# Performance work log

Measured on AMD Instinct MI355X. Metric: run time of the kernel, lower is better.

## Reference

```python
import jax, jax.numpy as jnp
import numpy as np


def _soft_attention(h, context, W_in, W_out):
    """Luong soft-dot attention. h: [B,H], context: [B,L,H].
    W_in: [H,H] (in,out layout), W_out: [2H,H]."""
    target = h @ W_in                                  # [B, H]
    attn = jnp.einsum('blh,bh->bl', context, target)   # [B, L]
    p = jax.nn.softmax(attn, axis=-1)                  # [B, L]
    weighted_ctx = jnp.einsum('bl,blh->bh', p, context)  # [B, H]
    h_tilde = jnp.tanh(jnp.concatenate([weighted_ctx, h], axis=1) @ W_out)  # [B, H]
    return h_tilde, p


def setup_inputs() -> dict:
    key = jax.random.key(0)
    ks = jax.random.split(key, 13)
    B, L, H = 64, 512, 1024
    s2 = 1.0 / np.sqrt(2 * H)
    s1 = 1.0 / np.sqrt(H)
    return {
        'h_tilde_s': jax.random.normal(ks[0], (B, H), jnp.float32),
        'h_tilde_o': jax.random.normal(ks[1], (B, H), jnp.float32),
        'h_tilde_a': jax.random.normal(ks[2], (B, H), jnp.float32),
        'enc_out': jax.random.normal(ks[3], (B, L, H), jnp.float32),
        'full_feature_len': 36,
        'W_as': jax.random.normal(ks[4], (2 * H, H), jnp.float32) * s2,
        'W_so': jax.random.normal(ks[5], (2 * H, H), jnp.float32) * s2,
        'W_oa': jax.random.normal(ks[6], (2 * H, H), jnp.float32) * s2,
        'Win_as': jax.random.normal(ks[7], (H, H), jnp.float32) * s1,
        'Win_so': jax.random.normal(ks[8], (H, H), jnp.float32) * s1,
        'Win_oa': jax.random.normal(ks[9], (H, H), jnp.float32) * s1,
        'Wout_as': jax.random.normal(ks[10], (2 * H, H), jnp.float32) * s2,
        'Wout_so': jax.random.normal(ks[11], (2 * H, H), jnp.float32) * s2,
        'Wout_oa': jax.random.normal(ks[12], (2 * H, H), jnp.float32) * s2,
    }


def reference(h_tilde_s, h_tilde_o, h_tilde_a, enc_out, full_feature_len,
              W_as, W_so, W_oa, Win_as, Win_so, Win_oa,
              Wout_as, Wout_so, Wout_oa):
    # Relational contexts via concat + linear(no bias) + tanh
    h_as = jnp.tanh(jnp.concatenate([h_tilde_a, h_tilde_s], axis=1) @ W_as)  # [B,H]
    h_so = jnp.tanh(jnp.concatenate([h_tilde_s, h_tilde_o], axis=1) @ W_so)
    h_oa = jnp.tanh(jnp.concatenate([h_tilde_o, h_tilde_a], axis=1) @ W_oa)
    # Three parallel soft-dot attentions over encoder output
    sa_as, _ = _soft_attention(h_as, enc_out, Win_as, Wout_as)
    sa_so, _ = _soft_attention(h_so, enc_out, Win_so, Wout_so)
    sa_oa, _ = _soft_attention(h_oa, enc_out, Win_oa, Wout_oa)
    B, H = sa_as.shape
    F = full_feature_len
    # repeat_interleave of size-1 dim == broadcast tile to [B, F, H]
    ctx_mas = jnp.broadcast_to(sa_as[:, None, :], (B, F, H))
    ctx_mso = jnp.broadcast_to(sa_so[:, None, :], (B, F, H))
    ctx_moa = jnp.broadcast_to(sa_oa[:, None, :], (B, F, H))
    return (ctx_mas, ctx_mso, ctx_moa)
```

## Files before the change

kernel.cpp:

```cpp
#include <hip/hip_runtime.h>

constexpr int BB = 64;
constexpr int LL = 512;
constexpr int HH = 1024;
constexpr int SPLITK = 4;

struct Ptr3 { const float* p[3]; };

template<int K0, int K1>
__global__ __launch_bounds__(256)
void gemm_skinny(Ptr3 A0, Ptr3 A1, Ptr3 Wp, float* __restrict__ part)
{
    constexpr int K = K0 + K1;
    constexpr int KRANGE = K / SPLITK;
    __shared__ float As[32][64];
    __shared__ float Ws[32][64];
    const int r   = blockIdx.z;
    const int n0  = blockIdx.x * 64;
    const int ks  = blockIdx.y * KRANGE;
    const int tid = threadIdx.x;
    const float* a0 = A0.p[r];
    const float* a1 = A1.p[r];
    const float* w  = Wp.p[r];

    const int tn = tid & 15;
    const int tm = tid >> 4;

    float acc[4][4] = {};

    for (int kt = ks; kt < ks + KRANGE; kt += 32) {
        {
            const int m   = tid >> 2;
            const int kk0 = (tid & 3) << 3;
            const int kg  = kt + kk0;
            const float* src = (kg < K0) ? (a0 + m * HH + kg)
                                         : (a1 + m * HH + (kg - K0));
            float4 v0 = *(const float4*)(src);
            float4 v1 = *(const float4*)(src + 4);
            As[kk0 + 0][m] = v0.x; As[kk0 + 1][m] = v0.y;
            As[kk0 + 2][m] = v0.z; As[kk0 + 3][m] = v0.w;
            As[kk0 + 4][m] = v1.x; As[kk0 + 5][m] = v1.y;
            As[kk0 + 6][m] = v1.z; As[kk0 + 7][m] = v1.w;
        }
        {
            const int j4 = (tid & 15) << 2;
            int kk = tid >> 4;
            #pragma unroll
            for (int i = 0; i < 2; i++, kk += 16) {
                *(float4*)&Ws[kk][j4] = *(const float4*)(w + (size_t)(kt + kk) * HH + n0 + j4);
            }
        }
        __syncthreads();
        #pragma unroll
        for (int kk = 0; kk < 32; kk++) {
            float4 a4 = *(const float4*)&As[kk][tm << 2];
            float4 b4 = *(const float4*)&Ws[kk][tn << 2];
            float av[4] = {a4.x, a4.y, a4.z, a4.w};
            float bv[4] = {b4.x, b4.y, b4.z, b4.w};
            #pragma unroll
            for (int i = 0; i < 4; i++)
                #pragma unroll
                for (int j = 0; j < 4; j++)
                    acc[i][j] += av[i] * bv[j];
        }
        __syncthreads();
    }

    float* dst = part + (size_t)((r * SPLITK + blockIdx.y) * 64) * HH + n0 + (tn << 2);
    #pragma unroll
    for (int i = 0; i < 4; i++) {
        const int m = (tm << 2) + i;
        *(float4*)(dst + (size_t)m * HH) = make_float4(acc[i][0], acc[i][1], acc[i][2], acc[i][3]);
    }
}

template<bool TANH>
__global__ __launch_bounds__(256)
void reduce_split(const float* __restrict__ part, float* __restrict__ dst)
{
    const int i4   = blockIdx.x * 256 + threadIdx.x;
    const int flat = i4 << 2;
    const int r    = flat >> 16;
    const int mn   = flat & 65535;
    const float* p = part + (size_t)r * SPLITK * 65536 + mn;
    float4 s = *(const float4*)p;
    #pragma unroll
    for (int y = 1; y < SPLITK; y++) {
        float4 q = *(const float4*)(p + (size_t)y * 65536);
        s.x += q.x; s.y += q.y; s.z += q.z; s.w += q.w;
    }
    if (TANH) {
        s.x = tanhf(s.x); s.y = tanhf(s.y); s.z = tanhf(s.z); s.w = tanhf(s.w);
    }
    *(float4*)(dst + (size_t)r * 65536 + mn) = s;
}

__global__ __launch_bounds__(256)
void attn_scores(const float* __restrict__ enc, const float* __restrict__ t,
                 float* __restrict__ attn)
{
    const int b    = blockIdx.x >> 4;
    const int lc   = blockIdx.x & 15;
    const int lane = threadIdx.x & 63;
    const int wave = threadIdx.x >> 6;

    float4 tr[3][4];
    #pragma unroll
    for (int r = 0; r < 3; r++)
        #pragma unroll
        for (int v = 0; v < 4; v++)
            tr[r][v] = *(const float4*)&t[(size_t)(r * BB + b) * HH + (lane << 2) + (v << 8)];

    const int lbase = (lc << 5) + (wave << 3);
    for (int i = 0; i < 8; i++) {
        const int l = lbase + i;
        const float* e = enc + (size_t)(b * LL + l) * HH;
        float a0 = 0.f, a1 = 0.f, a2 = 0.f;
        #pragma unroll
        for (int v = 0; v < 4; v++) {
            float4 ev = *(const float4*)&e[(lane << 2) + (v << 8)];
            a0 += ev.x * tr[0][v].x + ev.y * tr[0][v].y + ev.z * tr[0][v].z + ev.w * tr[0][v].w;
            a1 += ev.x * tr[1][v].x + ev.y * tr[1][v].y + ev.z * tr[1][v].z + ev.w * tr[1][v].w;
            a2 += ev.x * tr[2][v].x + ev.y * tr[2][v].y + ev.z * tr[2][v].z + ev.w * tr[2][v].w;
        }
        #pragma unroll
        for (int off = 32; off > 0; off >>= 1) {
            a0 += __shfl_xor(a0, off);
            a1 += __shfl_xor(a1, off);
            a2 += __shfl_xor(a2, off);
        }
        if (lane == 0) {
            attn[(size_t)(0 * BB + b) * LL + l] = a0;
            attn[(size_t)(1 * BB + b) * LL + l] = a1;
            attn[(size_t)(2 * BB + b) * LL + l] = a2;
        }
    }
}

__global__ __launch_bounds__(256)
void wctx_softmax(const float* __restrict__ enc, const float* __restrict__ attn,
                  float* __restrict__ wctx)
{
    __shared__ float p[3][LL];
    __shared__ float red[256];
    const int b   = blockIdx.x;
    const int hc  = blockIdx.y;
    const int tid = threadIdx.x;

    #pragma unroll
    for (int r = 0; r < 3; r++) {
        float2 v = *(const float2*)&attn[(size_t)(r * BB + b) * LL + tid * 2];
        *(float2*)&p[r][tid * 2] = v;
    }
    __syncthreads();

    #pragma unroll
    for (int r = 0; r < 3; r++) {
        const float v0 = p[r][tid];
        const float v1 = p[r][tid + 256];
        red[tid] = fmaxf(v0, v1);
        __syncthreads();
        for (int s = 128; s > 0; s >>= 1) {
            if (tid < s) red[tid] = fmaxf(red[tid], red[tid + s]);
            __syncthreads();
        }
        const float m = red[0];
        __syncthreads();
        const float e0 = __expf(v0 - m);
        const float e1 = __expf(v1 - m);
        red[tid] = e0 + e1;
        __syncthreads();
        for (int s = 128; s > 0; s >>= 1) {
            if (tid < s) red[tid] += red[tid + s];
            __syncthreads();
        }
        const float inv = 1.0f / red[0];
        __syncthreads();
        p[r][tid]       = e0 * inv;
        p[r][tid + 256] = e1 * inv;
        __syncthreads();
    }

    const int h = (hc << 8) + tid;
    const float* e = enc + (size_t)b * LL * HH + h;
    float a0 = 0.f, a1 = 0.f, a2 = 0.f;
    #pragma unroll 8
    for (int l = 0; l < LL; l++) {
        const float ev = e[(size_t)l * HH];
        a0 += p[0][l] * ev;
        a1 += p[1][l] * ev;
        a2 += p[2][l] * ev;
    }
    wctx[(size_t)(0 * BB + b) * HH + h] = a0;
    wctx[(size_t)(1 * BB + b) * HH + h] = a1;
    wctx[(size_t)(2 * BB + b) * HH + h] = a2;
}

__global__ __launch_bounds__(256)
void reduce_tanh_broadcast(const float* __restrict__ part, const int* __restrict__ Fp,
                           float* __restrict__ out)
{
    const int i4   = blockIdx.x * 256 + threadIdx.x;
    const int flat = i4 << 2;
    const int r    = flat >> 16;
    const int mn   = flat & 65535;
    const float* p = part + (size_t)r * SPLITK * 65536 + mn;
    float4 s = *(const float4*)p;
    #pragma unroll
    for (int y = 1; y < SPLITK; y++) {
        float4 q = *(const float4*)(p + (size_t)y * 65536);
        s.x += q.x; s.y += q.y; s.z += q.z; s.w += q.w;
    }
    s.x = tanhf(s.x); s.y = tanhf(s.y); s.z = tanhf(s.z); s.w = tanhf(s.w);

    const int F  = *Fp;
    const int bb = mn >> 10;
    const int hh = mn & 1023;
    float* o = out + ((size_t)(r * BB + bb) * F) * HH + hh;
    for (int f = 0; f < F; f++)
        *(float4*)(o + (size_t)f * HH) = s;
}

extern "C" void kernel_launch(void* const* d_in, const int* in_sizes, int n_in,
                              void* d_out, int out_size, void* d_ws, size_t ws_size,
                              hipStream_t stream)
{
    (void)in_sizes; (void)n_in; (void)out_size; (void)ws_size;
    const float* hs  = (const float*)d_in[0];
    const float* ho  = (const float*)d_in[1];
    const float* ha  = (const float*)d_in[2];
    const float* enc = (const float*)d_in[3];
    const int*   Fp  = (const int*)d_in[4];
    const float* W_as    = (const float*)d_in[5];
    const float* W_so    = (const float*)d_in[6];
    const float* W_oa    = (const float*)d_in[7];
    const float* Win_as  = (const float*)d_in[8];
    const float* Win_so  = (const float*)d_in[9];
    const float* Win_oa  = (const float*)d_in[10];
    const float* Wout_as = (const float*)d_in[11];
    const float* Wout_so = (const float*)d_in[12];
    const float* Wout_oa = (const float*)d_in[13];

    float* ws   = (float*)d_ws;
    float* part = ws;
    float* hx   = ws + 786432;
    float* tt   = ws + 983040;
    float* at   = ws + 1179648;
    float* wc   = ws + 1277952;

    {
        Ptr3 A0{{ha, hs, ho}};
        Ptr3 A1{{hs, ho, ha}};
        Ptr3 W {{W_as, W_so, W_oa}};
        gemm_skinny<1024, 1024><<<dim3(16, SPLITK, 3), 256, 0, stream>>>(A0, A1, W, part);
    }
    reduce_split<true><<<192, 256, 0, stream>>>(part, hx);

    {
        Ptr3 A0{{hx, hx + 65536, hx + 131072}};
        Ptr3 A1{{nullptr, nullptr, nullptr}};
        Ptr3 W {{Win_as, Win_so, Win_oa}};
        gemm_skinny<1024, 0><<<dim3(16, SPLITK, 3), 256, 0, stream>>>(A0, A1, W, part);
    }
    reduce_split<false><<<192, 256, 0, stream>>>(part, tt);

    attn_scores<<<1024, 256, 0, stream>>>(enc, tt, at);

    wctx_softmax<<<dim3(64, 4), 256, 0, stream>>>(enc, at, wc);

    {
        Ptr3 A0{{wc, wc + 65536, wc + 131072}};
        Ptr3 A1{{hx, hx + 65536, hx + 131072}};
        Ptr3 W {{Wout_as, Wout_so, Wout_oa}};
        gemm_skinny<1024, 1024><<<dim3(16, SPLITK, 3), 256, 0, stream>>>(A0, A1, W, part);
    }

    reduce_tanh_broadcast<<<192, 256, 0, stream>>>(part, Fp, (float*)d_out);
}
```

Baseline: 370.0 us.

## Raise split-K, fuse partial reductions into consumers, split softmax and weighted-context passes

Split-K for the three skinny GEMMs goes from 4 to 16, giving 768 blocks instead of 192 to fill the GPU. The reduction of the Win GEMM partials is folded into attn_scores, and the 4-way L-split weighted-context partials are summed inside the output GEMM's A-tile load. Softmax becomes its own wave-per-row kernel. The weighted-context kernel is split over L with float4 loads and a shared-memory reduction, raising parallelism from 256 blocks. In exchange, partial-sum traffic rises (16 partials) and every attn_scores block re-reads 16 partials.

```diff
diff --git a/kernel.cpp b/kernel.cpp
--- a/kernel.cpp
+++ b/kernel.cpp
@@ -3,16 +3,17 @@
 constexpr int BB = 64;
 constexpr int LL = 512;
 constexpr int HH = 1024;
-constexpr int SPLITK = 4;
+constexpr int SPLITS = 16;
+constexpr int RSTRIDE = 3 * BB * HH;
 
 struct Ptr3 { const float* p[3]; };
 
-template<int K0, int K1>
+template<int K0, int K1, int NSUM0>
 __global__ __launch_bounds__(256)
 void gemm_skinny(Ptr3 A0, Ptr3 A1, Ptr3 Wp, float* __restrict__ part)
 {
     constexpr int K = K0 + K1;
-    constexpr int KRANGE = K / SPLITK;
+    constexpr int KRANGE = K / SPLITS;
     __shared__ float As[32][64];
     __shared__ float Ws[32][64];
     const int r   = blockIdx.z;
@@ -33,10 +34,23 @@
             const int m   = tid >> 2;
             const int kk0 = (tid & 3) << 3;
             const int kg  = kt + kk0;
-            const float* src = (kg < K0) ? (a0 + m * HH + kg)
-                                         : (a1 + m * HH + (kg - K0));
-            float4 v0 = *(const float4*)(src);
-            float4 v1 = *(const float4*)(src + 4);
+            float4 v0, v1;
+            if (K1 == 0 || kg < K0) {
+                const float* src = a0 + (size_t)m * HH + kg;
+                v0 = *(const float4*)(src);
+                v1 = *(const float4*)(src + 4);
+                #pragma unroll
+                for (int j = 1; j < NSUM0; j++) {
+                    float4 q0 = *(const float4*)(src + (size_t)j * RSTRIDE);
+                    float4 q1 = *(const float4*)(src + (size_t)j * RSTRIDE + 4);
+                    v0.x += q0.x; v0.y += q0.y; v0.z += q0.z; v0.w += q0.w;
+                    v1.x += q1.x; v1.y += q1.y; v1.z += q1.z; v1.w += q1.w;
+                }
+            } else {
+                const float* src = a1 + (size_t)m * HH + (kg - K0);
+                v0 = *(const float4*)(src);
+                v1 = *(const float4*)(src + 4);
+            }
             As[kk0 + 0][m] = v0.x; As[kk0 + 1][m] = v0.y;
             As[kk0 + 2][m] = v0.z; As[kk0 + 3][m] = v0.w;
             As[kk0 + 4][m] = v1.x; As[kk0 + 5][m] = v1.y;
@@ -66,7 +80,7 @@
         __syncthreads();
     }
 
-    float* dst = part + (size_t)((r * SPLITK + blockIdx.y) * 64) * HH + n0 + (tn << 2);
+    float* dst = part + (size_t)((r * SPLITS + blockIdx.y) * 64) * HH + n0 + (tn << 2);
     #pragma unroll
     for (int i = 0; i < 4; i++) {
         const int m = (tm << 2) + i;
@@ -74,29 +88,26 @@
     }
 }
 
-template<bool TANH>
-__global__ __launch_bounds__(256)
-void reduce_split(const float* __restrict__ part, float* __restrict__ dst)
+__global__ __launch_bounds__(256)
+void reduce_tanh(const float* __restrict__ part, float* __restrict__ dst)
 {
     const int i4   = blockIdx.x * 256 + threadIdx.x;
     const int flat = i4 << 2;
     const int r    = flat >> 16;
     const int mn   = flat & 65535;
-    const float* p = part + (size_t)r * SPLITK * 65536 + mn;
+    const float* p = part + (size_t)r * SPLITS * 65536 + mn;
     float4 s = *(const float4*)p;
     #pragma unroll
-    for (int y = 1; y < SPLITK; y++) {
+    for (int y = 1; y < SPLITS; y++) {
         float4 q = *(const float4*)(p + (size_t)y * 65536);
         s.x += q.x; s.y += q.y; s.z += q.z; s.w += q.w;
     }
-    if (TANH) {
-        s.x = tanhf(s.x); s.y = tanhf(s.y); s.z = tanhf(s.z); s.w = tanhf(s.w);
-    }
+    s.x = tanhf(s.x); s.y = tanhf(s.y); s.z = tanhf(s.z); s.w = tanhf(s.w);
     *(float4*)(dst + (size_t)r * 65536 + mn) = s;
 }
 
 __global__ __launch_bounds__(256)
-void attn_scores(const float* __restrict__ enc, const float* __restrict__ t,
+void attn_scores(const float* __restrict__ enc, const float* __restrict__ part,
                  float* __restrict__ attn)
 {
     const int b    = blockIdx.x >> 4;
@@ -106,10 +117,20 @@
 
     float4 tr[3][4];
     #pragma unroll
-    for (int r = 0; r < 3; r++)
-        #pragma unroll
-        for (int v = 0; v < 4; v++)
-            tr[r][v] = *(const float4*)&t[(size_t)(r * BB + b) * HH + (lane << 2) + (v << 8)];
+    for (int r = 0; r < 3; r++) {
+        #pragma unroll
+        for (int v = 0; v < 4; v++) tr[r][v] = make_float4(0.f, 0.f, 0.f, 0.f);
+        #pragma unroll
+        for (int y = 0; y < SPLITS; y++) {
+            const float* q = part + ((size_t)((r * SPLITS + y) * 64 + b)) * HH + (lane << 2);
+            #pragma unroll
+            for (int v = 0; v < 4; v++) {
+                float4 t4 = *(const float4*)(q + (v << 8));
+                tr[r][v].x += t4.x; tr[r][v].y += t4.y;
+                tr[r][v].z += t4.z; tr[r][v].w += t4.w;
+            }
+        }
+    }
 
     const int lbase = (lc << 5) + (wave << 3);
     for (int i = 0; i < 8; i++) {
@@ -137,63 +158,89 @@
     }
 }
 
-__global__ __launch_bounds__(256)
-void wctx_softmax(const float* __restrict__ enc, const float* __restrict__ attn,
-                  float* __restrict__ wctx)
-{
-    __shared__ float p[3][LL];
-    __shared__ float red[256];
-    const int b   = blockIdx.x;
-    const int hc  = blockIdx.y;
-    const int tid = threadIdx.x;
-
-    #pragma unroll
-    for (int r = 0; r < 3; r++) {
-        float2 v = *(const float2*)&attn[(size_t)(r * BB + b) * LL + tid * 2];
-        *(float2*)&p[r][tid * 2] = v;
-    }
+__global__ __launch_bounds__(64)
+void softmax_rows(const float* __restrict__ at, float* __restrict__ pn)
+{
+    const int row  = blockIdx.x;
+    const int lane = threadIdx.x;
+    const float* src = at + (size_t)row * LL + lane * 8;
+    float4 x0 = *(const float4*)src;
+    float4 x1 = *(const float4*)(src + 4);
+    float m = fmaxf(fmaxf(fmaxf(x0.x, x0.y), fmaxf(x0.z, x0.w)),
+                    fmaxf(fmaxf(x1.x, x1.y), fmaxf(x1.z, x1.w)));
+    #pragma unroll
+    for (int off = 32; off > 0; off >>= 1) m = fmaxf(m, __shfl_xor(m, off));
+    float4 e0, e1;
+    e0.x = __expf(x0.x - m); e0.y = __expf(x0.y - m);
+    e0.z = __expf(x0.z - m); e0.w = __expf(x0.w - m);
+    e1.x = __expf(x1.x - m); e1.y = __expf(x1.y - m);
+    e1.z = __expf(x1.z - m); e1.w = __expf(x1.w - m);
+    float s = e0.x + e0.y + e0.z + e0.w + e1.x + e1.y + e1.z + e1.w;
+    #pragma unroll
+    for (int off = 32; off > 0; off >>= 1) s += __shfl_xor(s, off);
+    const float inv = 1.0f / s;
+    e0.x *= inv; e0.y *= inv; e0.z *= inv; e0.w *= inv;
+    e1.x *= inv; e1.y *= inv; e1.z *= inv; e1.w *= inv;
+    float* dst = pn + (size_t)row * LL + lane * 8;
+    *(float4*)dst = e0;
+    *(float4*)(dst + 4) = e1;
+}
+
+__global__ __launch_bounds__(256)
+void wctx_partial(const float* __restrict__ enc, const float* __restrict__ pn,
+                  float* __restrict__ wcp)
+{
+    __shared__ float pl[3][128];
+    __shared__ float4 red[3][3][64];
+    const int b    = blockIdx.x;
+    const int hc   = blockIdx.y;
+    const int ls   = blockIdx.z;
+    const int tid  = threadIdx.x;
+    const int lane = tid & 63;
+    const int lg   = tid >> 6;
+
+    #pragma unroll
+    for (int r = 0; r < 3; r++)
+        if (tid < 128) pl[r][tid] = pn[(size_t)(r * BB + b) * LL + ls * 128 + tid];
     __syncthreads();
 
-    #pragma unroll
-    for (int r = 0; r < 3; r++) {
-        const float v0 = p[r][tid];
-        const float v1 = p[r][tid + 256];
-        red[tid] = fmaxf(v0, v1);
-        __syncthreads();
-        for (int s = 128; s > 0; s >>= 1) {
-            if (tid < s) red[tid] = fmaxf(red[tid], red[tid + s]);
-            __syncthreads();
-        }
-        const float m = red[0];
-        __syncthreads();
-        const float e0 = __expf(v0 - m);
-        const float e1 = __expf(v1 - m);
-        red[tid] = e0 + e1;
-        __syncthreads();
-        for (int s = 128; s > 0; s >>= 1) {
-            if (tid < s) red[tid] += red[tid + s];
-            __syncthreads();
-        }
-        const float inv = 1.0f / red[0];
-        __syncthreads();
-        p[r][tid]       = e0 * inv;
-        p[r][tid + 256] = e1 * inv;
-        __syncthreads();
-    }
-
-    const int h = (hc << 8) + tid;
-    const float* e = enc + (size_t)b * LL * HH + h;
-    float a0 = 0.f, a1 = 0.f, a2 = 0.f;
+    const int h = (hc << 8) + (lane << 2);
+    const float* e = enc + ((size_t)b * LL + ls * 128 + lg * 32) * HH + h;
+    float4 a0 = make_float4(0.f, 0.f, 0.f, 0.f);
+    float4 a1 = a0, a2 = a0;
     #pragma unroll 8
-    for (int l = 0; l < LL; l++) {
-        const float ev = e[(size_t)l * HH];
-        a0 += p[0][l] * ev;
-        a1 += p[1][l] * ev;
-        a2 += p[2][l] * ev;
-    }
-    wctx[(size_t)(0 * BB + b) * HH + h] = a0;
-    wctx[(size_t)(1 * BB + b) * HH + h] = a1;
-    wctx[(size_t)(2 * BB + b) * HH + h] = a2;
+    for (int i = 0; i < 32; i++) {
+        float4 ev = *(const float4*)(e + (size_t)i * HH);
+        const float q0 = pl[0][lg * 32 + i];
+        const float q1 = pl[1][lg * 32 + i];
+        const float q2 = pl[2][lg * 32 + i];
+        a0.x += ev.x * q0; a0.y += ev.y * q0; a0.z += ev.z * q0; a0.w += ev.w * q0;
+        a1.x += ev.x * q1; a1.y += ev.y * q1; a1.z += ev.z * q1; a1.w += ev.w * q1;
+        a2.x += ev.x * q2; a2.y += ev.y * q2; a2.z += ev.z * q2; a2.w += ev.w * q2;
+    }
+
+    if (lg > 0) {
+        red[lg - 1][0][lane] = a0;
+        red[lg - 1][1][lane] = a1;
+        red[lg - 1][2][lane] = a2;
+    }
+    __syncthreads();
+    if (lg == 0) {
+        #pragma unroll
+        for (int w = 0; w < 3; w++) {
+            float4 q;
+            q = red[w][0][lane];
+            a0.x += q.x; a0.y += q.y; a0.z += q.z; a0.w += q.w;
+            q = red[w][1][lane];
+            a1.x += q.x; a1.y += q.y; a1.z += q.z; a1.w += q.w;
+            q = red[w][2][lane];
+            a2.x += q.x; a2.y += q.y; a2.z += q.z; a2.w += q.w;
+        }
+        float* dst = wcp + (size_t)ls * RSTRIDE + (size_t)b * HH + h;
+        *(float4*)(dst + 0 * BB * HH) = a0;
+        *(float4*)(dst + 1 * BB * HH) = a1;
+        *(float4*)(dst + 2 * BB * HH) = a2;
+    }
 }
 
 __global__ __launch_bounds__(256)
@@ -204,10 +251,10 @@
     const int flat = i4 << 2;
     const int r    = flat >> 16;
     const int mn   = flat & 65535;
-    const float* p = part + (size_t)r * SPLITK * 65536 + mn;
+    const float* p = part + (size_t)r * SPLITS * 65536 + mn;
     float4 s = *(const float4*)p;
     #pragma unroll
-    for (int y = 1; y < SPLITK; y++) {
+    for (int y = 1; y < SPLITS; y++) {
         float4 q = *(const float4*)(p + (size_t)y * 65536);
         s.x += q.x; s.y += q.y; s.z += q.z; s.w += q.w;
     }
@@ -243,36 +290,37 @@
 
     float* ws   = (float*)d_ws;
     float* part = ws;
-    float* hx   = ws + 786432;
-    float* tt   = ws + 983040;
-    float* at   = ws + 1179648;
-    float* wc   = ws + 1277952;
+    float* hx   = ws + 3145728;
+    float* at   = ws + 3342336;
+    float* pn   = ws + 3440640;
+    float* wcp  = ws + 3538944;
 
     {
         Ptr3 A0{{ha, hs, ho}};
         Ptr3 A1{{hs, ho, ha}};
         Ptr3 W {{W_as, W_so, W_oa}};
-        gemm_skinny<1024, 1024><<<dim3(16, SPLITK, 3), 256, 0, stream>>>(A0, A1, W, part);
-    }
-    reduce_split<true><<<192, 256, 0, stream>>>(part, hx);
+        gemm_skinny<1024, 1024, 1><<<dim3(16, SPLITS, 3), 256, 0, stream>>>(A0, A1, W, part);
+    }
+    reduce_tanh<<<192, 256, 0, stream>>>(part, hx);
 
     {
         Ptr3 A0{{hx, hx + 65536, hx + 131072}};
         Ptr3 A1{{nullptr, nullptr, nullptr}};
         Ptr3 W {{Win_as, Win_so, Win_oa}};
-        gemm_skinny<1024, 0><<<dim3(16, SPLITK, 3), 256, 0, stream>>>(A0, A1, W, part);
-    }
-    reduce_split<false><<<192, 256, 0, stream>>>(part, tt);
-
-    attn_scores<<<1024, 256, 0, stream>>>(enc, tt, at);
-
-    wctx_softmax<<<dim3(64, 4), 256, 0, stream>>>(enc, at, wc);
+        gemm_skinny<1024, 0, 1><<<dim3(16, SPLITS, 3), 256, 0, stream>>>(A0, A1, W, part);
+    }
+
+    attn_scores<<<1024, 256, 0, stream>>>(enc, part, at);
+
+    softmax_rows<<<192, 64, 0, stream>>>(at, pn);
+
+    wctx_partial<<<dim3(64, 4, 4), 256, 0, stream>>>(enc, pn, wcp);
 
     {
-        Ptr3 A0{{wc, wc + 65536, wc + 131072}};
+        Ptr3 A0{{wcp, wcp + 65536, wcp + 131072}};
         Ptr3 A1{{hx, hx + 65536, hx + 131072}};
         Ptr3 W {{Wout_as, Wout_so, Wout_oa}};
-        gemm_skinny<1024, 1024><<<dim3(16, SPLITK, 3), 256, 0, stream>>>(A0, A1, W, part);
+        gemm_skinny<1024, 1024, 4><<<dim3(16, SPLITS, 3), 256, 0, stream>>>(A0, A1, W, part);
     }
 
     reduce_tanh_broadcast<<<192, 256, 0, stream>>>(part, Fp, (float*)d_out);
```

Measured after the change: 346.9 us. 6.2% less time.

## Fuse attention scores, softmax and weighted context into flash-style chunked pass

Applied to the files above, without the earlier changes.

Replaces the separate score kernel and the softmax-plus-weighted-context kernel with a flash-style chunk kernel. Each block holds 16 encoder rows in registers, computes scores, a local softmax and a partial weighted sum. A combine kernel then merges the per-chunk max and sum statistics. The encoder tensor is read once instead of twice, and the strided column read in the old weighted-context kernel goes away. Separately, split-K for the skinny GEMMs goes from 4 to 16 for more parallelism, at the cost of larger partial buffers and more reduction traffic.

```diff
diff --git a/kernel.cpp b/kernel.cpp
--- a/kernel.cpp
+++ b/kernel.cpp
@@ -3,7 +3,7 @@
 constexpr int BB = 64;
 constexpr int LL = 512;
 constexpr int HH = 1024;
-constexpr int SPLITK = 4;
+constexpr int SPLITS = 16;
 
 struct Ptr3 { const float* p[3]; };
 
@@ -12,7 +12,7 @@
 void gemm_skinny(Ptr3 A0, Ptr3 A1, Ptr3 Wp, float* __restrict__ part)
 {
     constexpr int K = K0 + K1;
-    constexpr int KRANGE = K / SPLITK;
+    constexpr int KRANGE = K / SPLITS;
     __shared__ float As[32][64];
     __shared__ float Ws[32][64];
     const int r   = blockIdx.z;
@@ -33,8 +33,8 @@
             const int m   = tid >> 2;
             const int kk0 = (tid & 3) << 3;
             const int kg  = kt + kk0;
-            const float* src = (kg < K0) ? (a0 + m * HH + kg)
-                                         : (a1 + m * HH + (kg - K0));
+            const float* src = (K1 == 0 || kg < K0) ? (a0 + (size_t)m * HH + kg)
+                                                    : (a1 + (size_t)m * HH + (kg - K0));
             float4 v0 = *(const float4*)(src);
             float4 v1 = *(const float4*)(src + 4);
             As[kk0 + 0][m] = v0.x; As[kk0 + 1][m] = v0.y;
@@ -66,7 +66,7 @@
         __syncthreads();
     }
 
-    float* dst = part + (size_t)((r * SPLITK + blockIdx.y) * 64) * HH + n0 + (tn << 2);
+    float* dst = part + (size_t)((r * SPLITS + blockIdx.y) * 64) * HH + n0 + (tn << 2);
     #pragma unroll
     for (int i = 0; i < 4; i++) {
         const int m = (tm << 2) + i;
@@ -82,10 +82,10 @@
     const int flat = i4 << 2;
     const int r    = flat >> 16;
     const int mn   = flat & 65535;
-    const float* p = part + (size_t)r * SPLITK * 65536 + mn;
+    const float* p = part + (size_t)r * SPLITS * 65536 + mn;
     float4 s = *(const float4*)p;
     #pragma unroll
-    for (int y = 1; y < SPLITK; y++) {
+    for (int y = 1; y < SPLITS; y++) {
         float4 q = *(const float4*)(p + (size_t)y * 65536);
         s.x += q.x; s.y += q.y; s.z += q.z; s.w += q.w;
     }
@@ -96,104 +96,136 @@
 }
 
 __global__ __launch_bounds__(256)
-void attn_scores(const float* __restrict__ enc, const float* __restrict__ t,
-                 float* __restrict__ attn)
-{
-    const int b    = blockIdx.x >> 4;
-    const int lc   = blockIdx.x & 15;
-    const int lane = threadIdx.x & 63;
-    const int wave = threadIdx.x >> 6;
+void flash_chunk(const float* __restrict__ enc, const float* __restrict__ tt,
+                 float* __restrict__ opm, float* __restrict__ ms)
+{
+    __shared__ float o_l[4][3][HH];
+    __shared__ float ms_sh[4][3][2];
+    const int b    = blockIdx.x >> 5;
+    const int lc   = blockIdx.x & 31;
+    const int tid  = threadIdx.x;
+    const int lane = tid & 63;
+    const int w    = tid >> 6;
 
     float4 tr[3][4];
     #pragma unroll
     for (int r = 0; r < 3; r++)
         #pragma unroll
         for (int v = 0; v < 4; v++)
-            tr[r][v] = *(const float4*)&t[(size_t)(r * BB + b) * HH + (lane << 2) + (v << 8)];
-
-    const int lbase = (lc << 5) + (wave << 3);
-    for (int i = 0; i < 8; i++) {
-        const int l = lbase + i;
-        const float* e = enc + (size_t)(b * LL + l) * HH;
-        float a0 = 0.f, a1 = 0.f, a2 = 0.f;
+            tr[r][v] = *(const float4*)&tt[(size_t)(r * BB + b) * HH + (lane << 2) + (v << 8)];
+
+    const int l0 = (lc << 4) + (w << 2);
+    const float* e = enc + ((size_t)b * LL + l0) * HH + (lane << 2);
+    float4 ev[4][4];
+    #pragma unroll
+    for (int j = 0; j < 4; j++)
+        #pragma unroll
+        for (int v = 0; v < 4; v++)
+            ev[j][v] = *(const float4*)(e + (size_t)j * HH + (v << 8));
+
+    float s[3][4];
+    #pragma unroll
+    for (int j = 0; j < 4; j++) {
+        float d0 = 0.f, d1 = 0.f, d2 = 0.f;
         #pragma unroll
         for (int v = 0; v < 4; v++) {
-            float4 ev = *(const float4*)&e[(lane << 2) + (v << 8)];
-            a0 += ev.x * tr[0][v].x + ev.y * tr[0][v].y + ev.z * tr[0][v].z + ev.w * tr[0][v].w;
-            a1 += ev.x * tr[1][v].x + ev.y * tr[1][v].y + ev.z * tr[1][v].z + ev.w * tr[1][v].w;
-            a2 += ev.x * tr[2][v].x + ev.y * tr[2][v].y + ev.z * tr[2][v].z + ev.w * tr[2][v].w;
+            const float4 x = ev[j][v];
+            d0 += x.x * tr[0][v].x + x.y * tr[0][v].y + x.z * tr[0][v].z + x.w * tr[0][v].w;
+            d1 += x.x * tr[1][v].x + x.y * tr[1][v].y + x.z * tr[1][v].z + x.w * tr[1][v].w;
+            d2 += x.x * tr[2][v].x + x.y * tr[2][v].y + x.z * tr[2][v].z + x.w * tr[2][v].w;
         }
         #pragma unroll
         for (int off = 32; off > 0; off >>= 1) {
-            a0 += __shfl_xor(a0, off);
-            a1 += __shfl_xor(a1, off);
-            a2 += __shfl_xor(a2, off);
-        }
-        if (lane == 0) {
-            attn[(size_t)(0 * BB + b) * LL + l] = a0;
-            attn[(size_t)(1 * BB + b) * LL + l] = a1;
-            attn[(size_t)(2 * BB + b) * LL + l] = a2;
-        }
-    }
-}
-
-__global__ __launch_bounds__(256)
-void wctx_softmax(const float* __restrict__ enc, const float* __restrict__ attn,
-                  float* __restrict__ wctx)
-{
-    __shared__ float p[3][LL];
-    __shared__ float red[256];
+            d0 += __shfl_xor(d0, off);
+            d1 += __shfl_xor(d1, off);
+            d2 += __shfl_xor(d2, off);
+        }
+        s[0][j] = d0; s[1][j] = d1; s[2][j] = d2;
+    }
+
+    #pragma unroll
+    for (int r = 0; r < 3; r++) {
+        const float m = fmaxf(fmaxf(s[r][0], s[r][1]), fmaxf(s[r][2], s[r][3]));
+        float p[4];
+        float sum = 0.f;
+        #pragma unroll
+        for (int j = 0; j < 4; j++) { p[j] = __expf(s[r][j] - m); sum += p[j]; }
+        #pragma unroll
+        for (int v = 0; v < 4; v++) {
+            float4 o = make_float4(0.f, 0.f, 0.f, 0.f);
+            #pragma unroll
+            for (int j = 0; j < 4; j++) {
+                const float4 x = ev[j][v];
+                o.x += p[j] * x.x; o.y += p[j] * x.y;
+                o.z += p[j] * x.z; o.w += p[j] * x.w;
+            }
+            *(float4*)&o_l[w][r][(lane << 2) + (v << 8)] = o;
+        }
+        if (lane == 0) { ms_sh[w][r][0] = m; ms_sh[w][r][1] = sum; }
+    }
+    __syncthreads();
+
+    const int chunk = (b << 5) + lc;
+    #pragma unroll
+    for (int r = 0; r < 3; r++) {
+        float m0 = ms_sh[0][r][0], m1 = ms_sh[1][r][0];
+        float m2 = ms_sh[2][r][0], m3 = ms_sh[3][r][0];
+        const float M = fmaxf(fmaxf(m0, m1), fmaxf(m2, m3));
+        const float w0 = __expf(m0 - M), w1 = __expf(m1 - M);
+        const float w2 = __expf(m2 - M), w3 = __expf(m3 - M);
+        float4 q0 = *(const float4*)&o_l[0][r][tid << 2];
+        float4 q1 = *(const float4*)&o_l[1][r][tid << 2];
+        float4 q2 = *(const float4*)&o_l[2][r][tid << 2];
+        float4 q3 = *(const float4*)&o_l[3][r][tid << 2];
+        float4 acc;
+        acc.x = w0 * q0.x + w1 * q1.x + w2 * q2.x + w3 * q3.x;
+        acc.y = w0 * q0.y + w1 * q1.y + w2 * q2.y + w3 * q3.y;
+        acc.z = w0 * q0.z + w1 * q1.z + w2 * q2.z + w3 * q3.z;
+        acc.w = w0 * q0.w + w1 * q1.w + w2 * q2.w + w3 * q3.w;
+        *(float4*)&opm[((size_t)chunk * 3 + r) * HH + (tid << 2)] = acc;
+        if (tid == 0) {
+            const float S = w0 * ms_sh[0][r][1] + w1 * ms_sh[1][r][1]
+                          + w2 * ms_sh[2][r][1] + w3 * ms_sh[3][r][1];
+            ms[((size_t)chunk * 3 + r) * 2 + 0] = M;
+            ms[((size_t)chunk * 3 + r) * 2 + 1] = S;
+        }
+    }
+}
+
+__global__ __launch_bounds__(256)
+void flash_combine(const float* __restrict__ opm, const float* __restrict__ ms,
+                   float* __restrict__ wc)
+{
+    __shared__ float ms_l[32][2];
     const int b   = blockIdx.x;
-    const int hc  = blockIdx.y;
+    const int r   = blockIdx.y;
     const int tid = threadIdx.x;
 
-    #pragma unroll
-    for (int r = 0; r < 3; r++) {
-        float2 v = *(const float2*)&attn[(size_t)(r * BB + b) * LL + tid * 2];
-        *(float2*)&p[r][tid * 2] = v;
+    if (tid < 32) {
+        const int chunk = (b << 5) + tid;
+        ms_l[tid][0] = ms[((size_t)chunk * 3 + r) * 2 + 0];
+        ms_l[tid][1] = ms[((size_t)chunk * 3 + r) * 2 + 1];
     }
     __syncthreads();
 
-    #pragma unroll
-    for (int r = 0; r < 3; r++) {
-        const float v0 = p[r][tid];
-        const float v1 = p[r][tid + 256];
-        red[tid] = fmaxf(v0, v1);
-        __syncthreads();
-        for (int s = 128; s > 0; s >>= 1) {
-            if (tid < s) red[tid] = fmaxf(red[tid], red[tid + s]);
-            __syncthreads();
-        }
-        const float m = red[0];
-        __syncthreads();
-        const float e0 = __expf(v0 - m);
-        const float e1 = __expf(v1 - m);
-        red[tid] = e0 + e1;
-        __syncthreads();
-        for (int s = 128; s > 0; s >>= 1) {
-            if (tid < s) red[tid] += red[tid + s];
-            __syncthreads();
-        }
-        const float inv = 1.0f / red[0];
-        __syncthreads();
-        p[r][tid]       = e0 * inv;
-        p[r][tid + 256] = e1 * inv;
-        __syncthreads();
-    }
-
-    const int h = (hc << 8) + tid;
-    const float* e = enc + (size_t)b * LL * HH + h;
-    float a0 = 0.f, a1 = 0.f, a2 = 0.f;
+    float M = -3.4e38f;
     #pragma unroll 8
-    for (int l = 0; l < LL; l++) {
-        const float ev = e[(size_t)l * HH];
-        a0 += p[0][l] * ev;
-        a1 += p[1][l] * ev;
-        a2 += p[2][l] * ev;
-    }
-    wctx[(size_t)(0 * BB + b) * HH + h] = a0;
-    wctx[(size_t)(1 * BB + b) * HH + h] = a1;
-    wctx[(size_t)(2 * BB + b) * HH + h] = a2;
+    for (int c = 0; c < 32; c++) M = fmaxf(M, ms_l[c][0]);
+
+    float S = 0.f;
+    float4 acc = make_float4(0.f, 0.f, 0.f, 0.f);
+    #pragma unroll 4
+    for (int c = 0; c < 32; c++) {
+        const float wgt = __expf(ms_l[c][0] - M);
+        S += wgt * ms_l[c][1];
+        const int chunk = (b << 5) + c;
+        float4 q = *(const float4*)&opm[((size_t)chunk * 3 + r) * HH + (tid << 2)];
+        acc.x += wgt * q.x; acc.y += wgt * q.y;
+        acc.z += wgt * q.z; acc.w += wgt * q.w;
+    }
+    const float inv = 1.0f / S;
+    acc.x *= inv; acc.y *= inv; acc.z *= inv; acc.w *= inv;
+    *(float4*)&wc[(size_t)(r * BB + b) * HH + (tid << 2)] = acc;
 }
 
 __global__ __launch_bounds__(256)
@@ -204,10 +236,10 @@
     const int flat = i4 << 2;
     const int r    = flat >> 16;
     const int mn   = flat & 65535;
-    const float* p = part + (size_t)r * SPLITK * 65536 + mn;
+    const float* p = part + (size_t)r * SPLITS * 65536 + mn;
     float4 s = *(const float4*)p;
     #pragma unroll
-    for (int y = 1; y < SPLITK; y++) {
+    for (int y = 1; y < SPLITS; y++) {
         float4 q = *(const float4*)(p + (size_t)y * 65536);
         s.x += q.x; s.y += q.y; s.z += q.z; s.w += q.w;
     }
@@ -243,16 +275,17 @@
 
     float* ws   = (float*)d_ws;
     float* part = ws;
-    float* hx   = ws + 786432;
-    float* tt   = ws + 983040;
-    float* at   = ws + 1179648;
-    float* wc   = ws + 1277952;
+    float* hx   = ws + 3145728;
+    float* tt   = ws + 3342336;
+    float* wc   = ws + 3538944;
+    float* opm  = ws + 3735552;
+    float* msb  = ws + 10027008;
 
     {
         Ptr3 A0{{ha, hs, ho}};
         Ptr3 A1{{hs, ho, ha}};
         Ptr3 W {{W_as, W_so, W_oa}};
-        gemm_skinny<1024, 1024><<<dim3(16, SPLITK, 3), 256, 0, stream>>>(A0, A1, W, part);
+        gemm_skinny<1024, 1024><<<dim3(16, SPLITS, 3), 256, 0, stream>>>(A0, A1, W, part);
     }
     reduce_split<true><<<192, 256, 0, stream>>>(part, hx);
 
@@ -260,19 +293,18 @@
         Ptr3 A0{{hx, hx + 65536, hx + 131072}};
         Ptr3 A1{{nullptr, nullptr, nullptr}};
         Ptr3 W {{Win_as, Win_so, Win_oa}};
-        gemm_skinny<1024, 0><<<dim3(16, SPLITK, 3), 256, 0, stream>>>(A0, A1, W, part);
+        gemm_skinny<1024, 0><<<dim3(16, SPLITS, 3), 256, 0, stream>>>(A0, A1, W, part);
     }
     reduce_split<false><<<192, 256, 0, stream>>>(part, tt);
 
-    attn_scores<<<1024, 256, 0, stream>>>(enc, tt, at);
-
-    wctx_softmax<<<dim3(64, 4), 256, 0, stream>>>(enc, at, wc);
+    flash_chunk<<<2048, 256, 0, stream>>>(enc, tt, opm, msb);
+    flash_combine<<<dim3(64, 3), 256, 0, stream>>>(opm, msb, wc);
 
     {
         Ptr3 A0{{wc, wc + 65536, wc + 131072}};
         Ptr3 A1{{hx, hx + 65536, hx + 131072}};
         Ptr3 W {{Wout_as, Wout_so, Wout_oa}};
-        gemm_skinny<1024, 1024><<<dim3(16, SPLITK, 3), 256, 0, stream>>>(A0, A1, W, part);
+        gemm_skinny<1024, 1024><<<dim3(16, SPLITS, 3), 256, 0, stream>>>(A0, A1, W, part);
     }
 
     reduce_tanh_broadcast<<<192, 256, 0, stream>>>(part, Fp, (float*)d_out);
```

New measurement: 323.4 us. -12.6%, faster.
